# Performance work log

Hardware: AMD Instinct MI355X
Metric: run time of the kernel (lower is better)

## Reference

```python
import jax, jax.numpy as jnp
import numpy as np
from numpy.polynomial import Polynomial

B, C = 2000000, 10
EXP = dict(start=0.0, stop=1.0, n=1000, deg=8)
INV = dict(start=10.0, stop=30.0, n=1000, deg=4)
LOG = dict(start=0.01, stop=0.5, n=1000, deg=8)
ITERATIONS = 3


def _fit(fn, start, stop, n, deg):
    x = np.linspace(start, stop, n)
    return Polynomial.fit(x, fn(x), deg).convert(kind=Polynomial).coef.astype(np.float32)


def _polyval(coeffs, x):
    # Horner; coeffs ascending order (numpy Polynomial convention)
    res = jnp.full_like(x, coeffs[-1])
    for i in range(coeffs.shape[0] - 2, -1, -1):
        res = res * x + coeffs[i]
    return res


def setup_inputs() -> dict:
    key = jax.random.key(0)
    k1, k2 = jax.random.split(key)
    enc_input = jax.random.uniform(k1, (B, C), dtype=jnp.float32)  # logits in [0,1)
    labels = jax.random.randint(k2, (B,), 0, C)
    enc_target = jax.nn.one_hot(labels, C, dtype=jnp.float32)
    exp_coeffs = jnp.asarray(_fit(np.exp, **{'start': EXP['start'], 'stop': EXP['stop'], 'n': EXP['n'], 'deg': EXP['deg']}))
    inverse_coeffs = jnp.asarray(_fit(lambda x: 1.0 / x, INV['start'], INV['stop'], INV['n'], INV['deg']))
    log_coeffs = jnp.asarray(_fit(np.log, LOG['start'], LOG['stop'], LOG['n'], LOG['deg']))
    return {
        'enc_input': enc_input,
        'enc_target': enc_target,
        'exp_coeffs': exp_coeffs,
        'inverse_coeffs': inverse_coeffs,
        'log_coeffs': log_coeffs,
        'iterations': ITERATIONS,
    }


def reference(enc_input, enc_target, exp_coeffs, inverse_coeffs, log_coeffs, iterations):
    # exp via polynomial approximation (Horner / ciphertext poly eval)
    e = _polyval(exp_coeffs, enc_input)                      # [B, C]
    s = jnp.sum(e, axis=1, keepdims=True)                    # [B, 1]
    # inverse via polynomial initial guess + Newton-Raphson refinement
    inv = _polyval(inverse_coeffs, s)
    for _ in range(iterations):
        inv = inv * (2.0 - s * inv)
    softmax = e * inv                                        # [B, C]
    log_softmax = _polyval(log_coeffs, softmax)              # [B, C]
    # mean cross-entropy over the batch
    loss = -jnp.sum(enc_target * log_softmax) / enc_input.shape[0]
    return loss


if __name__ == '__main__':
    out = reference(**setup_inputs())
    print(out)
```

## Files before the change

### kernel.cpp

```cpp
#include <hip/hip_runtime.h>

#define CCOL 10
#define TPB 256
#define PAIR_BYTES 80
#define WAVE_BYTES (64 * PAIR_BYTES)
#define CHUNK 1024

typedef const __attribute__((address_space(1))) void* gptr_t;
typedef __attribute__((address_space(3))) void* lptr_t;

__global__ void zero_kernel(float* out) {
    if (threadIdx.x == 0 && blockIdx.x == 0) out[0] = 0.0f;
}

__global__ __launch_bounds__(TPB) void ce_kernel(
    const float* __restrict__ x, const float* __restrict__ tgt,
    const float* __restrict__ exp_c, const float* __restrict__ inv_c,
    const float* __restrict__ log_c, const int* __restrict__ iters_p,
    float* __restrict__ out, int npairs, int full_blocks, float neg_inv_b)
{
    __shared__ float sx[TPB * 2 * CCOL];
    __shared__ float st[TPB * 2 * CCOL];

    float ec[9], ic[5], lc[9];
#pragma unroll
    for (int i = 0; i < 9; i++) ec[i] = exp_c[i];
#pragma unroll
    for (int i = 0; i < 5; i++) ic[i] = inv_c[i];
#pragma unroll
    for (int i = 0; i < 9; i++) lc[i] = log_c[i];
    const int niter = iters_p[0];

    const int tid  = threadIdx.x;
    const int lane = tid & 63;
    const int w    = tid >> 6;
    const int pair0 = blockIdx.x * TPB;

    float xr[2 * CCOL], tr[2 * CCOL];
    bool have = false;

    if (blockIdx.x < full_blocks) {
        const char* gx = (const char*)x   + (size_t)pair0 * PAIR_BYTES + w * WAVE_BYTES + lane * 16;
        const char* gt = (const char*)tgt + (size_t)pair0 * PAIR_BYTES + w * WAVE_BYTES + lane * 16;
        char* lx = (char*)sx + w * WAVE_BYTES + lane * 16;
        char* lt = (char*)st + w * WAVE_BYTES + lane * 16;
#pragma unroll
        for (int i = 0; i < 5; i++)
            __builtin_amdgcn_global_load_lds((gptr_t)(gx + i * CHUNK), (lptr_t)(lx + i * CHUNK), 16, 0, 0);
#pragma unroll
        for (int i = 0; i < 5; i++)
            __builtin_amdgcn_global_load_lds((gptr_t)(gt + i * CHUNK), (lptr_t)(lt + i * CHUNK), 16, 0, 0);
        __syncthreads();

        const float4* xv = (const float4*)(sx + tid * 2 * CCOL);
        const float4* tv = (const float4*)(st + tid * 2 * CCOL);
#pragma unroll
        for (int i = 0; i < 5; i++) {
            float4 v = xv[i];
            xr[4 * i + 0] = v.x; xr[4 * i + 1] = v.y;
            xr[4 * i + 2] = v.z; xr[4 * i + 3] = v.w;
        }
#pragma unroll
        for (int i = 0; i < 5; i++) {
            float4 v = tv[i];
            tr[4 * i + 0] = v.x; tr[4 * i + 1] = v.y;
            tr[4 * i + 2] = v.z; tr[4 * i + 3] = v.w;
        }
        have = true;
    } else {
        int p = pair0 + tid;
        if (p < npairs) {
            const float4* xv = (const float4*)(x   + (size_t)p * 2 * CCOL);
            const float4* tv = (const float4*)(tgt + (size_t)p * 2 * CCOL);
#pragma unroll
            for (int i = 0; i < 5; i++) {
                float4 v = xv[i];
                xr[4 * i + 0] = v.x; xr[4 * i + 1] = v.y;
                xr[4 * i + 2] = v.z; xr[4 * i + 3] = v.w;
            }
#pragma unroll
            for (int i = 0; i < 5; i++) {
                float4 v = tv[i];
                tr[4 * i + 0] = v.x; tr[4 * i + 1] = v.y;
                tr[4 * i + 2] = v.z; tr[4 * i + 3] = v.w;
            }
            have = true;
        }
    }

    float local = 0.0f;
    if (have) {
#pragma unroll
        for (int r = 0; r < 2; r++) {
            float e[CCOL];
            float s = 0.0f;
#pragma unroll
            for (int c = 0; c < CCOL; c++) {
                float xx = xr[r * CCOL + c];
                float v = ec[8];
#pragma unroll
                for (int i = 7; i >= 0; i--) v = fmaf(v, xx, ec[i]);
                e[c] = v;
                s += v;
            }
            float inv = ic[4];
#pragma unroll
            for (int i = 3; i >= 0; i--) inv = fmaf(inv, s, ic[i]);
            for (int k = 0; k < niter; k++) inv = inv * (2.0f - s * inv);

#pragma unroll
            for (int c = 0; c < CCOL; c++) {
                float sm = e[c] * inv;
                float v = lc[8];
#pragma unroll
                for (int i = 7; i >= 0; i--) v = fmaf(v, sm, lc[i]);
                local = fmaf(tr[r * CCOL + c], v, local);
            }
        }
    }

#pragma unroll
    for (int off = 32; off > 0; off >>= 1)
        local += __shfl_down(local, off, 64);

    __shared__ float wsum[4];
    if (lane == 0) wsum[w] = local;
    __syncthreads();
    if (tid == 0) {
        float b = wsum[0] + wsum[1] + wsum[2] + wsum[3];
        atomicAdd(out, b * neg_inv_b);
    }
}

extern "C" void kernel_launch(void* const* d_in, const int* in_sizes, int n_in,
                              void* d_out, int out_size, void* d_ws, size_t ws_size,
                              hipStream_t stream) {
    const float* x  = (const float*)d_in[0];
    const float* t  = (const float*)d_in[1];
    const float* ec = (const float*)d_in[2];
    const float* ic = (const float*)d_in[3];
    const float* lc = (const float*)d_in[4];
    const int*   it = (const int*)d_in[5];
    float* out = (float*)d_out;

    int b_rows = in_sizes[0] / CCOL;
    int npairs = b_rows / 2;
    float neg_inv_b = -1.0f / (float)b_rows;

    int full_blocks = npairs / TPB;
    int tail = npairs - full_blocks * TPB;
    int blocks = full_blocks + (tail ? 1 : 0);

    zero_kernel<<<1, 64, 0, stream>>>(out);
    ce_kernel<<<blocks, TPB, 0, stream>>>(x, t, ec, ic, lc, it, out,
                                          npairs, full_blocks, neg_inv_b);
}
```

Before: 190.6 us.

## Use persistent grid-stride blocks with two-stage deterministic reduction

Launches a fixed grid of 768 blocks that loop over 256-pair chunks instead of one block per chunk, writes per-block partial sums to the workspace, and reduces them in a second single-block kernel instead of using per-block atomics plus a zeroing kernel. This is meant to cut block launch overhead and remove about 3900 atomics on a single address. In exchange, the loop serialises each block's load-then-compute with no double buffering, so latency hiding now depends on how many blocks fit per CU, and a second __syncthreads is added per iteration.

After: 185.2 us. 1.03x faster.

```diff
diff --git a/kernel.cpp b/kernel.cpp
--- a/kernel.cpp
+++ b/kernel.cpp
@@ -4,20 +4,17 @@
 #define TPB 256
 #define PAIR_BYTES 80
 #define WAVE_BYTES (64 * PAIR_BYTES)
-#define CHUNK 1024
+#define CHUNK_LD 1024
+#define NBLOCKS 768
 
 typedef const __attribute__((address_space(1))) void* gptr_t;
 typedef __attribute__((address_space(3))) void* lptr_t;
-
-__global__ void zero_kernel(float* out) {
-    if (threadIdx.x == 0 && blockIdx.x == 0) out[0] = 0.0f;
-}
 
 __global__ __launch_bounds__(TPB) void ce_kernel(
     const float* __restrict__ x, const float* __restrict__ tgt,
     const float* __restrict__ exp_c, const float* __restrict__ inv_c,
     const float* __restrict__ log_c, const int* __restrict__ iters_p,
-    float* __restrict__ out, int npairs, int full_blocks, float neg_inv_b)
+    float* __restrict__ partials, int npairs, int full_chunks, int total_chunks)
 {
     __shared__ float sx[TPB * 2 * CCOL];
     __shared__ float st[TPB * 2 * CCOL];
@@ -34,44 +31,29 @@
     const int tid  = threadIdx.x;
     const int lane = tid & 63;
     const int w    = tid >> 6;
-    const int pair0 = blockIdx.x * TPB;
 
-    float xr[2 * CCOL], tr[2 * CCOL];
-    bool have = false;
+    float local = 0.0f;
 
-    if (blockIdx.x < full_blocks) {
-        const char* gx = (const char*)x   + (size_t)pair0 * PAIR_BYTES + w * WAVE_BYTES + lane * 16;
-        const char* gt = (const char*)tgt + (size_t)pair0 * PAIR_BYTES + w * WAVE_BYTES + lane * 16;
-        char* lx = (char*)sx + w * WAVE_BYTES + lane * 16;
-        char* lt = (char*)st + w * WAVE_BYTES + lane * 16;
+    for (int c = blockIdx.x; c < total_chunks; c += gridDim.x) {
+        const int pair0 = c * TPB;
+        float xr[2 * CCOL], tr[2 * CCOL];
+        bool have = false;
+
+        if (c < full_chunks) {
+            const char* gx = (const char*)x   + (size_t)pair0 * PAIR_BYTES + w * WAVE_BYTES + lane * 16;
+            const char* gt = (const char*)tgt + (size_t)pair0 * PAIR_BYTES + w * WAVE_BYTES + lane * 16;
+            char* lx = (char*)sx + w * WAVE_BYTES + lane * 16;
+            char* lt = (char*)st + w * WAVE_BYTES + lane * 16;
 #pragma unroll
-        for (int i = 0; i < 5; i++)
-            __builtin_amdgcn_global_load_lds((gptr_t)(gx + i * CHUNK), (lptr_t)(lx + i * CHUNK), 16, 0, 0);
+            for (int i = 0; i < 5; i++)
+                __builtin_amdgcn_global_load_lds((gptr_t)(gx + i * CHUNK_LD), (lptr_t)(lx + i * CHUNK_LD), 16, 0, 0);
 #pragma unroll
-        for (int i = 0; i < 5; i++)
-            __builtin_amdgcn_global_load_lds((gptr_t)(gt + i * CHUNK), (lptr_t)(lt + i * CHUNK), 16, 0, 0);
-        __syncthreads();
+            for (int i = 0; i < 5; i++)
+                __builtin_amdgcn_global_load_lds((gptr_t)(gt + i * CHUNK_LD), (lptr_t)(lt + i * CHUNK_LD), 16, 0, 0);
+            __syncthreads();
 
-        const float4* xv = (const float4*)(sx + tid * 2 * CCOL);
-        const float4* tv = (const float4*)(st + tid * 2 * CCOL);
-#pragma unroll
-        for (int i = 0; i < 5; i++) {
-            float4 v = xv[i];
-            xr[4 * i + 0] = v.x; xr[4 * i + 1] = v.y;
-            xr[4 * i + 2] = v.z; xr[4 * i + 3] = v.w;
-        }
-#pragma unroll
-        for (int i = 0; i < 5; i++) {
-            float4 v = tv[i];
-            tr[4 * i + 0] = v.x; tr[4 * i + 1] = v.y;
-            tr[4 * i + 2] = v.z; tr[4 * i + 3] = v.w;
-        }
-        have = true;
-    } else {
-        int p = pair0 + tid;
-        if (p < npairs) {
-            const float4* xv = (const float4*)(x   + (size_t)p * 2 * CCOL);
-            const float4* tv = (const float4*)(tgt + (size_t)p * 2 * CCOL);
+            const float4* xv = (const float4*)(sx + tid * 2 * CCOL);
+            const float4* tv = (const float4*)(st + tid * 2 * CCOL);
 #pragma unroll
             for (int i = 0; i < 5; i++) {
                 float4 v = xv[i];
@@ -84,37 +66,56 @@
                 tr[4 * i + 0] = v.x; tr[4 * i + 1] = v.y;
                 tr[4 * i + 2] = v.z; tr[4 * i + 3] = v.w;
             }
+            __syncthreads();
             have = true;
+        } else {
+            int p = pair0 + tid;
+            if (p < npairs) {
+                const float4* xv = (const float4*)(x   + (size_t)p * 2 * CCOL);
+                const float4* tv = (const float4*)(tgt + (size_t)p * 2 * CCOL);
+#pragma unroll
+                for (int i = 0; i < 5; i++) {
+                    float4 v = xv[i];
+                    xr[4 * i + 0] = v.x; xr[4 * i + 1] = v.y;
+                    xr[4 * i + 2] = v.z; xr[4 * i + 3] = v.w;
+                }
+#pragma unroll
+                for (int i = 0; i < 5; i++) {
+                    float4 v = tv[i];
+                    tr[4 * i + 0] = v.x; tr[4 * i + 1] = v.y;
+                    tr[4 * i + 2] = v.z; tr[4 * i + 3] = v.w;
+                }
+                have = true;
+            }
         }
-    }
 
-    float local = 0.0f;
-    if (have) {
+        if (have) {
 #pragma unroll
-        for (int r = 0; r < 2; r++) {
-            float e[CCOL];
-            float s = 0.0f;
+            for (int r = 0; r < 2; r++) {
+                float e[CCOL];
+                float s = 0.0f;
 #pragma unroll
-            for (int c = 0; c < CCOL; c++) {
-                float xx = xr[r * CCOL + c];
-                float v = ec[8];
+                for (int cc = 0; cc < CCOL; cc++) {
+                    float xx = xr[r * CCOL + cc];
+                    float v = ec[8];
 #pragma unroll
-                for (int i = 7; i >= 0; i--) v = fmaf(v, xx, ec[i]);
-                e[c] = v;
-                s += v;
-            }
-            float inv = ic[4];
+                    for (int i = 7; i >= 0; i--) v = fmaf(v, xx, ec[i]);
+                    e[cc] = v;
+                    s += v;
+                }
+                float inv = ic[4];
 #pragma unroll
-            for (int i = 3; i >= 0; i--) inv = fmaf(inv, s, ic[i]);
-            for (int k = 0; k < niter; k++) inv = inv * (2.0f - s * inv);
+                for (int i = 3; i >= 0; i--) inv = fmaf(inv, s, ic[i]);
+                for (int k = 0; k < niter; k++) inv = inv * (2.0f - s * inv);
 
 #pragma unroll
-            for (int c = 0; c < CCOL; c++) {
-                float sm = e[c] * inv;
-                float v = lc[8];
+                for (int cc = 0; cc < CCOL; cc++) {
+                    float sm = e[cc] * inv;
+                    float v = lc[8];
 #pragma unroll
-                for (int i = 7; i >= 0; i--) v = fmaf(v, sm, lc[i]);
-                local = fmaf(tr[r * CCOL + c], v, local);
+                    for (int i = 7; i >= 0; i--) v = fmaf(v, sm, lc[i]);
+                    local = fmaf(tr[r * CCOL + cc], v, local);
+                }
             }
         }
     }
@@ -126,10 +127,23 @@
     __shared__ float wsum[4];
     if (lane == 0) wsum[w] = local;
     __syncthreads();
-    if (tid == 0) {
-        float b = wsum[0] + wsum[1] + wsum[2] + wsum[3];
-        atomicAdd(out, b * neg_inv_b);
-    }
+    if (tid == 0)
+        partials[blockIdx.x] = wsum[0] + wsum[1] + wsum[2] + wsum[3];
+}
+
+__global__ __launch_bounds__(TPB) void reduce_kernel(
+    const float* __restrict__ partials, float* __restrict__ out, float neg_inv_b)
+{
+    int tid = threadIdx.x;
+    float local = partials[tid] + partials[tid + 256] + partials[tid + 512];
+#pragma unroll
+    for (int off = 32; off > 0; off >>= 1)
+        local += __shfl_down(local, off, 64);
+    __shared__ float wsum[4];
+    if ((tid & 63) == 0) wsum[tid >> 6] = local;
+    __syncthreads();
+    if (tid == 0)
+        out[0] = (wsum[0] + wsum[1] + wsum[2] + wsum[3]) * neg_inv_b;
 }
 
 extern "C" void kernel_launch(void* const* d_in, const int* in_sizes, int n_in,
@@ -142,16 +156,16 @@
     const float* lc = (const float*)d_in[4];
     const int*   it = (const int*)d_in[5];
     float* out = (float*)d_out;
+    float* partials = (float*)d_ws;
 
     int b_rows = in_sizes[0] / CCOL;
     int npairs = b_rows / 2;
     float neg_inv_b = -1.0f / (float)b_rows;
 
-    int full_blocks = npairs / TPB;
-    int tail = npairs - full_blocks * TPB;
-    int blocks = full_blocks + (tail ? 1 : 0);
+    int full_chunks  = npairs / TPB;
+    int total_chunks = full_chunks + (npairs % TPB ? 1 : 0);
 
-    zero_kernel<<<1, 64, 0, stream>>>(out);
-    ce_kernel<<<blocks, TPB, 0, stream>>>(x, t, ec, ic, lc, it, out,
-                                          npairs, full_blocks, neg_inv_b);
+    ce_kernel<<<NBLOCKS, TPB, 0, stream>>>(x, t, ec, ic, lc, it, partials,
+                                           npairs, full_chunks, total_chunks);
+    reduce_kernel<<<1, TPB, 0, stream>>>(partials, out, neg_inv_b);
 }
```
